# Kernel optimization log

Hardware: AMD Instinct MI355X
Metric: run time of the kernel (lower is better)

## Reference

```python
import jax, jax.numpy as jnp
import numpy as np

N_NODES = 50000  # 4 node types x 12500
N_PER = 12500
E = 600000
H = 128
IN_DIMS = [128, 128, 64, 64]


def setup_inputs() -> dict:
    key = jax.random.key(0)
    ks = jax.random.split(key, 16)
    inp = {}
    for i, d in enumerate(IN_DIMS):
        inp[f"feat{i}"] = jax.random.normal(ks[i], (N_PER, d), dtype=jnp.float32)
        # xavier_normal-ish init, gain 1.414
        std = 1.414 * np.sqrt(2.0 / (d + H))
        inp[f"W_fc{i}"] = jax.random.normal(ks[4 + i], (d, H), dtype=jnp.float32) * std
        inp[f"b_fc{i}"] = jnp.zeros((H,), dtype=jnp.float32)
    inp["src"] = jax.random.randint(ks[8], (E,), 0, N_NODES, dtype=jnp.int32)
    inp["dst"] = jax.random.randint(ks[9], (E,), 0, N_NODES, dtype=jnp.int32)
    inp["e_feat"] = jax.random.randint(ks[10], (E,), 0, 36, dtype=jnp.int32)
    inp["b_g0"] = jnp.zeros((H,), dtype=jnp.float32)  # GraphConv layer0 (weight=False, bias)
    inp["W_g1"] = jax.random.normal(ks[11], (H, H), dtype=jnp.float32) * np.sqrt(1.0 / H)
    inp["b_g1"] = jnp.zeros((H,), dtype=jnp.float32)
    return inp


def _degree_norms(src, dst):
    ones = jnp.ones((src.shape[0],), dtype=jnp.float32)
    deg_out = jax.ops.segment_sum(ones, src, num_segments=N_NODES)
    deg_in = jax.ops.segment_sum(ones, dst, num_segments=N_NODES)
    # DGL norm='both': D_out^{-1/2} on src side, D_in^{-1/2} on dst side (clamp 0-degree)
    out_norm = jax.lax.rsqrt(jnp.maximum(deg_out, 1.0))
    in_norm = jax.lax.rsqrt(jnp.maximum(deg_in, 1.0))
    return out_norm, in_norm


def _gcn_aggregate(h, src, dst, out_norm, in_norm):
    m = (h * out_norm[:, None])[src]                      # [E, H] gather
    agg = jax.ops.segment_sum(m, dst, num_segments=N_NODES)
    return agg * in_norm[:, None]


def reference(feat0, feat1, feat2, feat3,
              W_fc0, b_fc0, W_fc1, b_fc1, W_fc2, b_fc2, W_fc3, b_fc3,
              src, dst, e_feat, b_g0, W_g1, b_g1):
    # per-node-type linear projections, then concat along node dim
    h = jnp.concatenate([
        feat0 @ W_fc0 + b_fc0,
        feat1 @ W_fc1 + b_fc1,
        feat2 @ W_fc2 + b_fc2,
        feat3 @ W_fc3 + b_fc3,
    ], axis=0)  # [N_NODES, H]

    out_norm, in_norm = _degree_norms(src, dst)
    # GraphConv layer 0: weight=False, bias, activation (dropout p=0 -> identity)
    h = jax.nn.relu(_gcn_aggregate(h, src, dst, out_norm, in_norm) + b_g0)
    # GraphConv layer 1: aggregate, then linear weight + bias, activation
    h = jax.nn.relu(_gcn_aggregate(h, src, dst, out_norm, in_norm) @ W_g1 + b_g1)

    e = e_feat.astype(jnp.float32)  # e_feat.reshape(-1,1).float() in original
    # forward graph: msg = ft + sum_{r in 0..4} where(e==r, ft, 0) = ft * (1 + 1{e in 0..4})
    w_fwd = 1.0 + sum((e == float(r)).astype(jnp.float32) for r in (0, 1, 2, 3, 4))
    agg_a = jax.ops.segment_sum(h[src] * w_fwd[:, None], dst, num_segments=N_NODES)
    # transpose graph (reversed edges, same e): msg = sum_{r in {6,14,30}} where(e==r, ft, 0)
    w_bwd = sum((e == float(r)).astype(jnp.float32) for r in (6, 14, 30))
    agg_b = jax.ops.segment_sum(h[dst] * w_bwd[:, None], src, num_segments=N_NODES)
    return agg_a + agg_b
```

## Files before the change

### kernel.cpp

```cpp
#include <hip/hip_runtime.h>
#include <hip/hip_bf16.h>

#define N_NODES 50000
#define N_PER   12500
#define E_EDGES 600000
#define HDIM    128

#define NBLK_BUILD ((E_EDGES + 255) / 256)
#define NBLK_FC    ((N_PER + 63) / 64)
#define BK_CAP  32
#define BKB_CAP 8
#define MASK31  0x7fffffff

typedef __attribute__((ext_vector_type(8))) short bfrag;
typedef __attribute__((ext_vector_type(4))) float ffrag;

__device__ __forceinline__ unsigned short f2bf(float f) {
    union { float f; unsigned u; } x; x.f = f;
    unsigned r = x.u + 0x7fffu + ((x.u >> 16) & 1u);
    return (unsigned short)(r >> 16);
}
__device__ __forceinline__ float lo_bf(unsigned v) { return __uint_as_float(v << 16); }
__device__ __forceinline__ float hi_bf(unsigned v) { return __uint_as_float(v & 0xffff0000u); }
__device__ __forceinline__ unsigned pack2(float a, float b) {
    return (unsigned)f2bf(a) | ((unsigned)f2bf(b) << 16);
}
__device__ __forceinline__ float onrm_of(int deg) {
    return rsqrtf(fmaxf((float)deg, 1.0f));
}

__device__ __forceinline__ void acc8_add(float* acc, uint4 v) {
    acc[0] += lo_bf(v.x); acc[1] += hi_bf(v.x);
    acc[2] += lo_bf(v.y); acc[3] += hi_bf(v.y);
    acc[4] += lo_bf(v.z); acc[5] += hi_bf(v.z);
    acc[6] += lo_bf(v.w); acc[7] += hi_bf(v.w);
}
__device__ __forceinline__ void acc8_addw(float* acc, uint4 v, float w) {
    acc[0] += lo_bf(v.x) * w; acc[1] += hi_bf(v.x) * w;
    acc[2] += lo_bf(v.y) * w; acc[3] += hi_bf(v.y) * w;
    acc[4] += lo_bf(v.z) * w; acc[5] += hi_bf(v.z) * w;
    acc[6] += lo_bf(v.w) * w; acc[7] += hi_bf(v.w) * w;
}

__global__ __launch_bounds__(256) void prep_kernel(
    const float* __restrict__ W0, const float* __restrict__ W1,
    const float* __restrict__ W2, const float* __restrict__ W3,
    const float* __restrict__ Wg,
    unsigned short* __restrict__ Wp, int* __restrict__ initp) {
    int b = blockIdx.x;
    if (b < 32) {
        int tid = b * 256 + threadIdx.x;
        const float* W; int D, base, off;
        if      (tid < 2048) { W = W0; D = 128; base = 0;    off = 0;     }
        else if (tid < 4096) { W = W1; D = 128; base = 2048; off = 16384; }
        else if (tid < 5120) { W = W2; D = 64;  base = 4096; off = 32768; }
        else if (tid < 6144) { W = W3; D = 64;  base = 5120; off = 40960; }
        else                 { W = Wg; D = 128; base = 6144; off = 49152; }
        int t2 = tid - base;
        int KT = D / 32;
        int l = t2 & 63;
        int tt = t2 >> 6;
        int kt = tt % KT, n0 = tt / KT;
        int n = n0 * 16 + (l & 15);
        int kb = kt * 32 + (l >> 4) * 8;
#pragma unroll
        for (int j = 0; j < 8; ++j)
            Wp[(size_t)off + (size_t)t2 * 8 + j] = f2bf(W[(size_t)(kb + j) * 128 + n]);
    } else {
        int blk = b - 32;
#pragma unroll
        for (int k = 0; k < 4; ++k) {
            int i = blk * 1024 + k * 256 + threadIdx.x;
            if (i < 5 * N_NODES)
                initp[i] = (i < 2 * N_NODES) ? -1 : 0;
        }
    }
}

template<int D>
__device__ __forceinline__ void fc_body(
    int blk, int tid,
    const float* __restrict__ X,
    const unsigned short* __restrict__ Wp,
    const float* __restrict__ bias,
    unsigned short* __restrict__ outbf,
    int rows)
{
    constexpr int KT = D / 32;
    const int lane = tid & 63;
    const int wave = tid >> 6;
    const int m = lane & 15, q = lane >> 4;
    const int rbase = blk * 64 + wave * 16;
    const int row = rbase + m;

    bfrag afr[KT];
#pragma unroll
    for (int kt = 0; kt < KT; ++kt) {
        bfrag a;
        if (row < rows) {
            const float* xp = X + (size_t)row * D + kt * 32 + q * 8;
            float4 u0 = *(const float4*)xp;
            float4 u1 = *(const float4*)(xp + 4);
            a[0] = (short)f2bf(u0.x); a[1] = (short)f2bf(u0.y);
            a[2] = (short)f2bf(u0.z); a[3] = (short)f2bf(u0.w);
            a[4] = (short)f2bf(u1.x); a[5] = (short)f2bf(u1.y);
            a[6] = (short)f2bf(u1.z); a[7] = (short)f2bf(u1.w);
        } else {
#pragma unroll
            for (int t = 0; t < 8; ++t) a[t] = 0;
        }
        afr[kt] = a;
    }

    ffrag acc[8];
#pragma unroll
    for (int n0 = 0; n0 < 8; ++n0)
#pragma unroll
        for (int t = 0; t < 4; ++t) acc[n0][t] = 0.f;

#pragma unroll
    for (int n0 = 0; n0 < 8; ++n0)
#pragma unroll
        for (int kt = 0; kt < KT; ++kt) {
            bfrag bfr = *(const bfrag*)(Wp + ((size_t)(n0 * KT + kt) * 64 + lane) * 8);
            acc[n0] = __builtin_amdgcn_mfma_f32_16x16x32_bf16(afr[kt], bfr, acc[n0], 0, 0, 0);
        }

#pragma unroll
    for (int n0 = 0; n0 < 8; ++n0) {
        const int col = n0 * 16 + m;
        const float bj = bias[col];
#pragma unroll
        for (int r = 0; r < 4; ++r) {
            int orow = rbase + q * 4 + r;
            if (orow < rows)
                outbf[(size_t)orow * 128 + col] = f2bf(acc[n0][r] + bj);
        }
    }
}

__global__ __launch_bounds__(256) void mega_kernel(
    const int* __restrict__ src, const int* __restrict__ dst,
    const int* __restrict__ ef,
    int* __restrict__ cnt_in, int* __restrict__ cntB,
    int* __restrict__ deg_out,
    int* __restrict__ bucket, int* __restrict__ bucketB,
    int* __restrict__ head_ov, int* __restrict__ ov_pay, int* __restrict__ ov_nxt,
    int* __restrict__ head_ovB, int* __restrict__ ovB_pay, int* __restrict__ ovB_nxt,
    const float* __restrict__ f0, const float* __restrict__ f1,
    const float* __restrict__ f2, const float* __restrict__ f3,
    const unsigned short* __restrict__ Wp,
    const float* __restrict__ b0, const float* __restrict__ b1,
    const float* __restrict__ b2, const float* __restrict__ b3,
    unsigned short* __restrict__ Abf)
{
    const int b = blockIdx.x;
    if (b < NBLK_BUILD) {
        int e = b * 256 + threadIdx.x;
        if (e >= E_EDGES) return;
        int s = src[e], d = dst[e], t = ef[e];
        int v = s | ((t <= 4) ? 0x80000000 : 0);
        int p = atomicAdd(&cnt_in[d], 1);
        if (p < BK_CAP) bucket[d * BK_CAP + p] = v;
        else { ov_pay[e] = v; ov_nxt[e] = atomicExch(&head_ov[d], e); }
        atomicAdd(&deg_out[s], 1);
        if (t == 6 || t == 14 || t == 30) {
            int p2 = atomicAdd(&cntB[s], 1);
            if (p2 < BKB_CAP) bucketB[s * BKB_CAP + p2] = d;
            else { ovB_pay[e] = d; ovB_nxt[e] = atomicExch(&head_ovB[s], e); }
        }
    } else {
        int fb = b - NBLK_BUILD;
        int which = fb / NBLK_FC;
        int blk = fb - which * NBLK_FC;
        if (which == 0)
            fc_body<128>(blk, threadIdx.x, f0, Wp,         b0, Abf + (size_t)0 * N_PER * HDIM, N_PER);
        else if (which == 1)
            fc_body<128>(blk, threadIdx.x, f1, Wp + 16384, b1, Abf + (size_t)1 * N_PER * HDIM, N_PER);
        else if (which == 2)
            fc_body<64>(blk, threadIdx.x, f2, Wp + 32768, b2, Abf + (size_t)2 * N_PER * HDIM, N_PER);
        else
            fc_body<64>(blk, threadIdx.x, f3, Wp + 40960, b3, Abf + (size_t)3 * N_PER * HDIM, N_PER);
    }
}

__global__ __launch_bounds__(256) void scale_kernel(
    uint4* __restrict__ A, const int* __restrict__ deg_out) {
    int idx = blockIdx.x * blockDim.x + threadIdx.x;
    int n = idx >> 4, j8 = idx & 15;
    float on = onrm_of(deg_out[n]);
    uint4 v = A[(size_t)n * 16 + j8];
    uint4 o;
    o.x = pack2(lo_bf(v.x) * on, hi_bf(v.x) * on);
    o.y = pack2(lo_bf(v.y) * on, hi_bf(v.y) * on);
    o.z = pack2(lo_bf(v.z) * on, hi_bf(v.z) * on);
    o.w = pack2(lo_bf(v.w) * on, hi_bf(v.w) * on);
    A[(size_t)n * 16 + j8] = o;
}

__global__ __launch_bounds__(256) void agg0_kernel(
    const uint4* __restrict__ A,
    const int* __restrict__ bucket, const int* __restrict__ cnt_in,
    const int* __restrict__ head_ov, const int* __restrict__ ov_pay,
    const int* __restrict__ ov_nxt,
    const int* __restrict__ deg_out, const float* __restrict__ b_g0,
    uint4* __restrict__ B) {
    int idx = blockIdx.x * blockDim.x + threadIdx.x;
    int n = idx >> 4, j8 = idx & 15;
    const int cnt = cnt_in[n];
    const int* bk = bucket + (size_t)n * BK_CAP;
    float acc[8] = {0.f, 0.f, 0.f, 0.f, 0.f, 0.f, 0.f, 0.f};
    int lim = min(cnt, BK_CAP);
    int i = 0;
    for (; i + 4 <= lim; i += 4) {
        int s0 = bk[i] & MASK31,     s1 = bk[i + 1] & MASK31;
        int s2 = bk[i + 2] & MASK31, s3 = bk[i + 3] & MASK31;
        uint4 v0 = A[(size_t)s0 * 16 + j8];
        uint4 v1 = A[(size_t)s1 * 16 + j8];
        uint4 v2 = A[(size_t)s2 * 16 + j8];
        uint4 v3 = A[(size_t)s3 * 16 + j8];
        acc8_add(acc, v0); acc8_add(acc, v1);
        acc8_add(acc, v2); acc8_add(acc, v3);
    }
    for (; i < lim; ++i) {
        int s = bk[i] & MASK31;
        acc8_add(acc, A[(size_t)s * 16 + j8]);
    }
    if (cnt > BK_CAP) {
        int e = head_ov[n];
        while (e >= 0) {
            int s = ov_pay[e] & MASK31;
            acc8_add(acc, A[(size_t)s * 16 + j8]);
            e = ov_nxt[e];
        }
    }
    float inr = onrm_of(cnt);
    float onr = onrm_of(deg_out[n]);
    const float* bg = b_g0 + j8 * 8;
    float r[8];
#pragma unroll
    for (int k = 0; k < 8; ++k)
        r[k] = fmaxf(acc[k] * inr + bg[k], 0.f) * onr;
    uint4 o;
    o.x = pack2(r[0], r[1]); o.y = pack2(r[2], r[3]);
    o.z = pack2(r[4], r[5]); o.w = pack2(r[6], r[7]);
    B[(size_t)n * 16 + j8] = o;
}

__global__ __launch_bounds__(256) void gemm1_fused_kernel(
    const unsigned short* __restrict__ Bbf,
    const int* __restrict__ bucket, const int* __restrict__ cnt_in,
    const int* __restrict__ head_ov, const int* __restrict__ ov_pay,
    const int* __restrict__ ov_nxt,
    const unsigned short* __restrict__ Wp, const float* __restrict__ bias,
    unsigned short* __restrict__ outbf)
{
    const int lane = threadIdx.x & 63;
    const int wave = threadIdx.x >> 6;
    const int m = lane & 15, q = lane >> 4;
    const int rbase = blockIdx.x * 64 + wave * 16;
    const int node = rbase + m;

    float ga[32];
#pragma unroll
    for (int i = 0; i < 32; ++i) ga[i] = 0.f;

    if (node < N_NODES) {
        const int cnt = cnt_in[node];
        const int* bk = bucket + (size_t)node * BK_CAP;
        int lim = min(cnt, BK_CAP);
        int i = 0;
        for (; i + 2 <= lim; i += 2) {
            int s0 = bk[i] & MASK31, s1 = bk[i + 1] & MASK31;
            const uint4* r0 = (const uint4*)(Bbf + (size_t)s0 * 128);
            const uint4* r1 = (const uint4*)(Bbf + (size_t)s1 * 128);
            uint4 a0 = r0[0 * 4 + q], a1 = r0[1 * 4 + q], a2 = r0[2 * 4 + q], a3 = r0[3 * 4 + q];
            uint4 c0 = r1[0 * 4 + q], c1 = r1[1 * 4 + q], c2 = r1[2 * 4 + q], c3 = r1[3 * 4 + q];
            acc8_add(ga +  0, a0); acc8_add(ga +  8, a1);
            acc8_add(ga + 16, a2); acc8_add(ga + 24, a3);
            acc8_add(ga +  0, c0); acc8_add(ga +  8, c1);
            acc8_add(ga + 16, c2); acc8_add(ga + 24, c3);
        }
        for (; i < lim; ++i) {
            int s = bk[i] & MASK31;
            const uint4* rp = (const uint4*)(Bbf + (size_t)s * 128);
#pragma unroll
            for (int kt = 0; kt < 4; ++kt) acc8_add(ga + kt * 8, rp[kt * 4 + q]);
        }
        if (cnt > BK_CAP) {
            int e = head_ov[node];
            while (e >= 0) {
                int s = ov_pay[e] & MASK31;
                const uint4* rp = (const uint4*)(Bbf + (size_t)s * 128);
#pragma unroll
                for (int kt = 0; kt < 4; ++kt) acc8_add(ga + kt * 8, rp[kt * 4 + q]);
                e = ov_nxt[e];
            }
        }
    }

    bfrag afr[4];
#pragma unroll
    for (int kt = 0; kt < 4; ++kt)
#pragma unroll
        for (int j = 0; j < 8; ++j)
            afr[kt][j] = (short)f2bf(ga[kt * 8 + j]);

    ffrag acc[8];
#pragma unroll
    for (int n0 = 0; n0 < 8; ++n0)
#pragma unroll
        for (int t = 0; t < 4; ++t) acc[n0][t] = 0.f;

#pragma unroll
    for (int n0 = 0; n0 < 8; ++n0)
#pragma unroll
        for (int kt = 0; kt < 4; ++kt) {
            bfrag bfr = *(const bfrag*)(Wp + ((size_t)(n0 * 4 + kt) * 64 + lane) * 8);
            acc[n0] = __builtin_amdgcn_mfma_f32_16x16x32_bf16(afr[kt], bfr, acc[n0], 0, 0, 0);
        }

    float ir[4];
#pragma unroll
    for (int r = 0; r < 4; ++r) {
        int orow = rbase + q * 4 + r;
        ir[r] = (orow < N_NODES) ? onrm_of(cnt_in[orow]) : 0.f;
    }
#pragma unroll
    for (int n0 = 0; n0 < 8; ++n0) {
        const int col = n0 * 16 + m;
        const float bj = bias[col];
#pragma unroll
        for (int r = 0; r < 4; ++r) {
            int orow = rbase + q * 4 + r;
            if (orow < N_NODES)
                outbf[(size_t)orow * 128 + col] = f2bf(fmaxf(acc[n0][r] * ir[r] + bj, 0.f));
        }
    }
}

__global__ __launch_bounds__(256) void final_kernel(
    const uint4* __restrict__ H,
    const int* __restrict__ bucket, const int* __restrict__ cnt_in,
    const int* __restrict__ head_ov, const int* __restrict__ ov_pay,
    const int* __restrict__ ov_nxt,
    const int* __restrict__ bucketB, const int* __restrict__ cntB,
    const int* __restrict__ head_ovB, const int* __restrict__ ovB_pay,
    const int* __restrict__ ovB_nxt,
    float4* __restrict__ out4) {
    int idx = blockIdx.x * blockDim.x + threadIdx.x;
    int n = idx >> 4, j8 = idx & 15;
    float acc[8] = {0.f, 0.f, 0.f, 0.f, 0.f, 0.f, 0.f, 0.f};
    const int cnt = cnt_in[n];
    const int* bk = bucket + (size_t)n * BK_CAP;
    int lim = min(cnt, BK_CAP);
    int i = 0;
    for (; i + 4 <= lim; i += 4) {
        int c0 = bk[i], c1 = bk[i + 1], c2 = bk[i + 2], c3 = bk[i + 3];
        uint4 v0 = H[(size_t)(c0 & MASK31) * 16 + j8];
        uint4 v1 = H[(size_t)(c1 & MASK31) * 16 + j8];
        uint4 v2 = H[(size_t)(c2 & MASK31) * 16 + j8];
        uint4 v3 = H[(size_t)(c3 & MASK31) * 16 + j8];
        acc8_addw(acc, v0, (c0 < 0) ? 2.0f : 1.0f);
        acc8_addw(acc, v1, (c1 < 0) ? 2.0f : 1.0f);
        acc8_addw(acc, v2, (c2 < 0) ? 2.0f : 1.0f);
        acc8_addw(acc, v3, (c3 < 0) ? 2.0f : 1.0f);
    }
    for (; i < lim; ++i) {
        int c = bk[i];
        acc8_addw(acc, H[(size_t)(c & MASK31) * 16 + j8], (c < 0) ? 2.0f : 1.0f);
    }
    if (cnt > BK_CAP) {
        int e = head_ov[n];
        while (e >= 0) {
            int c = ov_pay[e];
            acc8_addw(acc, H[(size_t)(c & MASK31) * 16 + j8], (c < 0) ? 2.0f : 1.0f);
            e = ov_nxt[e];
        }
    }
    const int cb = cntB[n];
    const int* bkB = bucketB + (size_t)n * BKB_CAP;
    int limB = min(cb, BKB_CAP);
    for (int k = 0; k < limB; ++k) {
        int d = bkB[k];
        acc8_add(acc, H[(size_t)d * 16 + j8]);
    }
    if (cb > BKB_CAP) {
        int e = head_ovB[n];
        while (e >= 0) {
            acc8_add(acc, H[(size_t)ovB_pay[e] * 16 + j8]);
            e = ovB_nxt[e];
        }
    }
    float4 o0 = {acc[0], acc[1], acc[2], acc[3]};
    float4 o1 = {acc[4], acc[5], acc[6], acc[7]};
    out4[(size_t)n * 32 + j8 * 2]     = o0;
    out4[(size_t)n * 32 + j8 * 2 + 1] = o1;
}

extern "C" void kernel_launch(void* const* d_in, const int* in_sizes, int n_in,
                              void* d_out, int out_size, void* d_ws, size_t ws_size,
                              hipStream_t stream) {
    const float* feat[4]  = {(const float*)d_in[0], (const float*)d_in[3],
                             (const float*)d_in[6], (const float*)d_in[9]};
    const float* W_fc[4]  = {(const float*)d_in[1], (const float*)d_in[4],
                             (const float*)d_in[7], (const float*)d_in[10]};
    const float* b_fc[4]  = {(const float*)d_in[2], (const float*)d_in[5],
                             (const float*)d_in[8], (const float*)d_in[11]};
    const int*   src      = (const int*)d_in[12];
    const int*   dst      = (const int*)d_in[13];
    const int*   efeat    = (const int*)d_in[14];
    const float* b_g0     = (const float*)d_in[15];
    const float* W_g1     = (const float*)d_in[16];
    const float* b_g1     = (const float*)d_in[17];
    float* out = (float*)d_out;

    char* p = (char*)d_ws;
    unsigned short* Abf = (unsigned short*)p; p += (size_t)N_NODES * HDIM * 2;
    unsigned short* Bbf = (unsigned short*)p; p += (size_t)N_NODES * HDIM * 2;
    unsigned short* Wp  = (unsigned short*)p; p += (size_t)65536 * 2;
    int* bucket  = (int*)p; p += (size_t)N_NODES * BK_CAP * 4;
    int* bucketB = (int*)p; p += (size_t)N_NODES * BKB_CAP * 4;
    int* ov_pay  = (int*)p; p += (size_t)E_EDGES * 4;
    int* ov_nxt  = (int*)p; p += (size_t)E_EDGES * 4;
    int* ovB_pay = (int*)p; p += (size_t)E_EDGES * 4;
    int* ovB_nxt = (int*)p; p += (size_t)E_EDGES * 4;
    int* head_ov  = (int*)p; p += (size_t)N_NODES * 4;
    int* head_ovB = (int*)p; p += (size_t)N_NODES * 4;
    int* cnt_in   = (int*)p; p += (size_t)N_NODES * 4;
    int* cntB     = (int*)p; p += (size_t)N_NODES * 4;
    int* deg_out  = (int*)p; p += (size_t)N_NODES * 4;

    const unsigned short* Wpg = Wp + 49152;

    prep_kernel<<<32 + (5 * N_NODES + 1023) / 1024, 256, 0, stream>>>(
        W_fc[0], W_fc[1], W_fc[2], W_fc[3], W_g1, Wp, head_ov);

    mega_kernel<<<NBLK_BUILD + 4 * NBLK_FC, 256, 0, stream>>>(
        src, dst, efeat, cnt_in, cntB, deg_out,
        bucket, bucketB, head_ov, ov_pay, ov_nxt, head_ovB, ovB_pay, ovB_nxt,
        feat[0], feat[1], feat[2], feat[3], Wp,
        b_fc[0], b_fc[1], b_fc[2], b_fc[3], Abf);

    const int grid_node = (N_NODES * 16) / 256;

    scale_kernel<<<grid_node, 256, 0, stream>>>((uint4*)Abf, deg_out);

    agg0_kernel<<<grid_node, 256, 0, stream>>>(
        (const uint4*)Abf, bucket, cnt_in, head_ov, ov_pay, ov_nxt,
        deg_out, b_g0, (uint4*)Bbf);

    gemm1_fused_kernel<<<(N_NODES + 63) / 64, 256, 0, stream>>>(
        Bbf, bucket, cnt_in, head_ov, ov_pay, ov_nxt, Wpg, b_g1, Abf);

    final_kernel<<<grid_node, 256, 0, stream>>>(
        (const uint4*)Abf, bucket, cnt_in, head_ov, ov_pay, ov_nxt,
        bucketB, cntB, head_ovB, ovB_pay, ovB_nxt, (float4*)out);
}
```

Before: 276.4 us.

## Compute out-degree via per-block LDS histograms instead of global atomics

Out-degree counting moves out of the edge-build kernel's global atomicAdd into prep_kernel. There, 128 blocks each build an LDS histogram for one quarter of the node range over one of 32 edge slices and write 16-bit partial counts. scale_kernel reduces the 32 partials per node with shuffles, computes the out-norm once and stores it for agg0. This removes 600k global atomics, at the cost of extra histogram blocks that each rescan an edge slice plus a partial-count buffer to read back.

```diff
diff --git a/kernel.cpp b/kernel.cpp
--- a/kernel.cpp
+++ b/kernel.cpp
@@ -12,6 +12,10 @@
 #define BKB_CAP 8
 #define MASK31  0x7fffffff
 
+#define HQ 32
+#define HP 4
+#define HSLICE (E_EDGES / HQ)
+
 typedef __attribute__((ext_vector_type(8))) short bfrag;
 typedef __attribute__((ext_vector_type(4))) float ffrag;
 
@@ -46,10 +50,28 @@
     const float* __restrict__ W0, const float* __restrict__ W1,
     const float* __restrict__ W2, const float* __restrict__ W3,
     const float* __restrict__ Wg,
-    unsigned short* __restrict__ Wp, int* __restrict__ initp) {
+    const int* __restrict__ src,
+    unsigned short* __restrict__ Wp, int* __restrict__ initp,
+    unsigned short* __restrict__ partial) {
+    __shared__ int hist[N_PER];
     int b = blockIdx.x;
-    if (b < 32) {
-        int tid = b * 256 + threadIdx.x;
+    if (b < HQ * HP) {
+        const int q = b >> 2;
+        const int p = b & 3;
+        for (int j = threadIdx.x; j < N_PER; j += 256) hist[j] = 0;
+        __syncthreads();
+        const int e0 = q * HSLICE;
+        for (int i = e0 + threadIdx.x; i < e0 + HSLICE; i += 256) {
+            int s = src[i];
+            unsigned r = (unsigned)(s - p * N_PER);
+            if (r < (unsigned)N_PER) atomicAdd(&hist[r], 1);
+        }
+        __syncthreads();
+        unsigned short* out = partial + (size_t)q * N_NODES + (size_t)p * N_PER;
+        for (int j = threadIdx.x; j < N_PER; j += 256)
+            out[j] = (unsigned short)hist[j];
+    } else if (b < HQ * HP + 32) {
+        int tid = (b - HQ * HP) * 256 + threadIdx.x;
         const float* W; int D, base, off;
         if      (tid < 2048) { W = W0; D = 128; base = 0;    off = 0;     }
         else if (tid < 4096) { W = W1; D = 128; base = 2048; off = 16384; }
@@ -67,11 +89,11 @@
         for (int j = 0; j < 8; ++j)
             Wp[(size_t)off + (size_t)t2 * 8 + j] = f2bf(W[(size_t)(kb + j) * 128 + n]);
     } else {
-        int blk = b - 32;
+        int blk = b - (HQ * HP + 32);
 #pragma unroll
         for (int k = 0; k < 4; ++k) {
             int i = blk * 1024 + k * 256 + threadIdx.x;
-            if (i < 5 * N_NODES)
+            if (i < 4 * N_NODES)
                 initp[i] = (i < 2 * N_NODES) ? -1 : 0;
         }
     }
@@ -143,7 +165,6 @@
     const int* __restrict__ src, const int* __restrict__ dst,
     const int* __restrict__ ef,
     int* __restrict__ cnt_in, int* __restrict__ cntB,
-    int* __restrict__ deg_out,
     int* __restrict__ bucket, int* __restrict__ bucketB,
     int* __restrict__ head_ov, int* __restrict__ ov_pay, int* __restrict__ ov_nxt,
     int* __restrict__ head_ovB, int* __restrict__ ovB_pay, int* __restrict__ ovB_nxt,
@@ -163,7 +184,6 @@
         int p = atomicAdd(&cnt_in[d], 1);
         if (p < BK_CAP) bucket[d * BK_CAP + p] = v;
         else { ov_pay[e] = v; ov_nxt[e] = atomicExch(&head_ov[d], e); }
-        atomicAdd(&deg_out[s], 1);
         if (t == 6 || t == 14 || t == 30) {
             int p2 = atomicAdd(&cntB[s], 1);
             if (p2 < BKB_CAP) bucketB[s * BKB_CAP + p2] = d;
@@ -185,10 +205,18 @@
 }
 
 __global__ __launch_bounds__(256) void scale_kernel(
-    uint4* __restrict__ A, const int* __restrict__ deg_out) {
+    uint4* __restrict__ A, const unsigned short* __restrict__ partial,
+    float* __restrict__ onrm_buf) {
     int idx = blockIdx.x * blockDim.x + threadIdx.x;
     int n = idx >> 4, j8 = idx & 15;
-    float on = onrm_of(deg_out[n]);
+    int d = (int)partial[(size_t)j8 * N_NODES + n]
+          + (int)partial[(size_t)(j8 + 16) * N_NODES + n];
+    d += __shfl_xor(d, 1);
+    d += __shfl_xor(d, 2);
+    d += __shfl_xor(d, 4);
+    d += __shfl_xor(d, 8);
+    float on = onrm_of(d);
+    if (j8 == 0) onrm_buf[n] = on;
     uint4 v = A[(size_t)n * 16 + j8];
     uint4 o;
     o.x = pack2(lo_bf(v.x) * on, hi_bf(v.x) * on);
@@ -203,7 +231,7 @@
     const int* __restrict__ bucket, const int* __restrict__ cnt_in,
     const int* __restrict__ head_ov, const int* __restrict__ ov_pay,
     const int* __restrict__ ov_nxt,
-    const int* __restrict__ deg_out, const float* __restrict__ b_g0,
+    const float* __restrict__ onrm_buf, const float* __restrict__ b_g0,
     uint4* __restrict__ B) {
     int idx = blockIdx.x * blockDim.x + threadIdx.x;
     int n = idx >> 4, j8 = idx & 15;
@@ -235,7 +263,7 @@
         }
     }
     float inr = onrm_of(cnt);
-    float onr = onrm_of(deg_out[n]);
+    float onr = onrm_buf[n];
     const float* bg = b_g0 + j8 * 8;
     float r[8];
 #pragma unroll
@@ -425,30 +453,32 @@
     int* ov_nxt  = (int*)p; p += (size_t)E_EDGES * 4;
     int* ovB_pay = (int*)p; p += (size_t)E_EDGES * 4;
     int* ovB_nxt = (int*)p; p += (size_t)E_EDGES * 4;
+    unsigned short* partial = (unsigned short*)p;
+    p += (size_t)HQ * N_NODES * 2;
+    float* onrm_buf = (float*)p; p += (size_t)N_NODES * 4;
     int* head_ov  = (int*)p; p += (size_t)N_NODES * 4;
     int* head_ovB = (int*)p; p += (size_t)N_NODES * 4;
     int* cnt_in   = (int*)p; p += (size_t)N_NODES * 4;
     int* cntB     = (int*)p; p += (size_t)N_NODES * 4;
-    int* deg_out  = (int*)p; p += (size_t)N_NODES * 4;
 
     const unsigned short* Wpg = Wp + 49152;
 
-    prep_kernel<<<32 + (5 * N_NODES + 1023) / 1024, 256, 0, stream>>>(
-        W_fc[0], W_fc[1], W_fc[2], W_fc[3], W_g1, Wp, head_ov);
+    prep_kernel<<<HQ * HP + 32 + (4 * N_NODES + 1023) / 1024, 256, 0, stream>>>(
+        W_fc[0], W_fc[1], W_fc[2], W_fc[3], W_g1, src, Wp, head_ov, partial);
 
     mega_kernel<<<NBLK_BUILD + 4 * NBLK_FC, 256, 0, stream>>>(
-        src, dst, efeat, cnt_in, cntB, deg_out,
+        src, dst, efeat, cnt_in, cntB,
         bucket, bucketB, head_ov, ov_pay, ov_nxt, head_ovB, ovB_pay, ovB_nxt,
         feat[0], feat[1], feat[2], feat[3], Wp,
         b_fc[0], b_fc[1], b_fc[2], b_fc[3], Abf);
 
     const int grid_node = (N_NODES * 16) / 256;
 
-    scale_kernel<<<grid_node, 256, 0, stream>>>((uint4*)Abf, deg_out);
+    scale_kernel<<<grid_node, 256, 0, stream>>>((uint4*)Abf, partial, onrm_buf);
 
     agg0_kernel<<<grid_node, 256, 0, stream>>>(
         (const uint4*)Abf, bucket, cnt_in, head_ov, ov_pay, ov_nxt,
-        deg_out, b_g0, (uint4*)Bbf);
+        onrm_buf, b_g0, (uint4*)Bbf);
 
     gemm1_fused_kernel<<<(N_NODES + 63) / 64, 256, 0, stream>>>(
         Bbf, bucket, cnt_in, head_ov, ov_pay, ov_nxt, Wpg, b_g1, Abf);
```

New measurement: 279.4 us. About the same (+1.1%).
